# Kernel tuning notes

Measured on AMD Instinct MI355X. Metric: run time of the kernel, lower is better.

The kernel has to match this reference:

```python
import jax, jax.numpy as jnp
import numpy as np

DIM = 2048
NUM_HEADS = 16
HEAD_DIM = DIM // NUM_HEADS  # 128
ROPE_BASE = 10000.0


def setup_inputs() -> dict:
    key = jax.random.key(0)
    k1, k2, k3 = jax.random.split(key, 3)
    B, S = 2, 2048
    x = jax.random.normal(k1, (B, S, DIM), dtype=jnp.float32)
    # causal mask: 1 where allowed (k <= q), 0 elsewhere
    mask = jnp.tril(jnp.ones((S, S), dtype=jnp.int32))
    # torch Linear(dim, 3*dim, bias=False): store transposed so y = x @ w
    w_qkv = jax.random.normal(k2, (DIM, 3 * DIM), dtype=jnp.float32) / np.sqrt(DIM)
    w_out = jax.random.normal(k3, (DIM, DIM), dtype=jnp.float32) / np.sqrt(DIM)
    return {"x": x, "w_qkv": w_qkv, "w_out": w_out, "mask": mask}


def _rope_cos_sin(seq_len, dtype):
    inv_freq = 1.0 / (ROPE_BASE ** (jnp.arange(0, HEAD_DIM, 2, dtype=jnp.float32) / HEAD_DIM))
    t = jnp.arange(seq_len, dtype=jnp.float32)
    freqs = t[:, None] * inv_freq[None, :]          # [S, D/2]
    emb = jnp.concatenate([freqs, freqs], axis=-1)  # [S, D]
    return jnp.cos(emb).astype(dtype), jnp.sin(emb).astype(dtype)


def _rotate_half(x):
    x1, x2 = jnp.split(x, 2, axis=-1)
    return jnp.concatenate([-x2, x1], axis=-1)


def reference(x, w_qkv, w_out, mask):
    B, S, _ = x.shape
    H, D = NUM_HEADS, HEAD_DIM
    qkv = x @ w_qkv                                   # [B, S, 3*dim]
    qkv = qkv.reshape(B, S, 3, H, D).transpose(2, 0, 3, 1, 4)  # [3, B, H, S, D]
    q, k, v = qkv[0], qkv[1], qkv[2]
    cos, sin = _rope_cos_sin(S, x.dtype)              # [S, D] broadcast over B,H
    q = q * cos + _rotate_half(q) * sin
    k = k * cos + _rotate_half(k) * sin
    scale = D ** -0.5
    score = jnp.einsum("bhqd,bhkd->bhqk", q, k) * scale
    score = jnp.where(mask == 0, -jnp.inf, score)
    attn = jax.nn.softmax(score, axis=-1)             # dropout = identity (eval)
    out = jnp.einsum("bhqk,bhkd->bhqd", attn, v)
    out = out.transpose(0, 2, 1, 3).reshape(B, S, H * D)
    return out @ w_out
```

## Files before the change

### kernel.cpp

```cpp
#include <hip/hip_runtime.h>

typedef __attribute__((ext_vector_type(8))) __bf16 bf16x8;
typedef __attribute__((ext_vector_type(4))) float f32x4;

__device__ __forceinline__ unsigned short f2bf(float x) {
  union { float f; unsigned int u; } v; v.f = x;
  unsigned int r = v.u + 0x7fffu + ((v.u >> 16) & 1u);
  return (unsigned short)(r >> 16);
}
__device__ __forceinline__ float bf2f(unsigned short x) {
  union { unsigned int u; float f; } v; v.u = ((unsigned int)x) << 16;
  return v.f;
}
__device__ __forceinline__ void g2l16(const void* g, void* l) {
  __builtin_amdgcn_global_load_lds((const __attribute__((address_space(1))) void*)g,
                                   (__attribute__((address_space(3))) void*)l, 16, 0, 0);
}

__global__ __launch_bounds__(256) void prep_k(const float* __restrict__ x,
                                              const float* __restrict__ wq,
                                              const float* __restrict__ wo,
                                              unsigned short* __restrict__ xb,
                                              unsigned short* __restrict__ wqT,
                                              unsigned short* __restrict__ woT) {
  __shared__ unsigned short t[64][65];
  const int b = blockIdx.x;
  if (b < 8192) {
    int i = b * 256 + threadIdx.x;
    float4 v = ((const float4*)x)[i];
    ushort4 o;
    o.x = f2bf(v.x); o.y = f2bf(v.y); o.z = f2bf(v.z); o.w = f2bf(v.w);
    ((ushort4*)xb)[i] = o;
    return;
  }
  const float* in; unsigned short* out; int C, c0, r0;
  const int R = 2048;
  if (b < 11264) { int bb = b - 8192;  in = wq; out = wqT; C = 6144; c0 = (bb % 96) * 64; r0 = (bb / 96) * 64; }
  else           { int bb = b - 11264; in = wo; out = woT; C = 2048; c0 = (bb & 31) * 64; r0 = (bb >> 5) * 64; }
  const int tx = threadIdx.x & 63, tg = threadIdx.x >> 6;
#pragma unroll
  for (int i = 0; i < 16; i++) {
    int r = i * 4 + tg;
    t[r][tx] = f2bf(in[(size_t)(r0 + r) * C + c0 + tx]);
  }
  __syncthreads();
#pragma unroll
  for (int i = 0; i < 16; i++) {
    int c = i * 4 + tg;
    out[(size_t)(c0 + c) * R + r0 + tx] = t[tx][c];
  }
}

template <int EPI>
__global__ __launch_bounds__(256) void gemm_bt_k(const unsigned short* __restrict__ A,
                                                 const unsigned short* __restrict__ BT,
                                                 int K, int N,
                                                 float* __restrict__ outF,
                                                 unsigned short* __restrict__ oq,
                                                 unsigned short* __restrict__ ok,
                                                 unsigned short* __restrict__ ov) {
  __shared__ __align__(16) unsigned short smem[17408];
  unsigned short* lA = smem;
  unsigned short* lB = smem + 8192;
  const int tid = threadIdx.x;
  const int w = tid >> 6, lane = tid & 63;
  const int quad = lane >> 4, l16 = lane & 15;
  const int m0 = blockIdx.y * 128, n0 = blockIdx.x * 128;
  const int wm = (w >> 1) * 64, wn = (w & 1) * 64;
  f32x4 acc[4][4] = {};
  const int srow = tid >> 3;
  const int schunk = (tid & 7) ^ (srow & 7);
  const unsigned short* gA = A + (size_t)(m0 + srow) * K + schunk * 8;
  const unsigned short* gB = BT + (size_t)(n0 + srow) * K + schunk * 8;
  char* ldA = (char*)lA + tid * 16;
  char* ldB = (char*)lB + tid * 16;
  const size_t rskip = (size_t)32 * K;
  for (int k0 = 0; k0 < K; k0 += 64) {
#pragma unroll
    for (int j = 0; j < 4; j++) {
      g2l16(gA + k0 + j * rskip, ldA + j * 4096);
      g2l16(gB + k0 + j * rskip, ldB + j * 4096);
    }
    __syncthreads();
#pragma unroll
    for (int ks = 0; ks < 2; ks++) {
      bf16x8 af[4], bfv[4];
#pragma unroll
      for (int i = 0; i < 4; i++)
        af[i] = *(const bf16x8*)((const char*)lA + (size_t)(wm + i * 16 + l16) * 128 +
                                 ((size_t)((ks * 4 + quad) ^ (l16 & 7)) * 16));
#pragma unroll
      for (int j = 0; j < 4; j++)
        bfv[j] = *(const bf16x8*)((const char*)lB + (size_t)(wn + j * 16 + l16) * 128 +
                                  ((size_t)((ks * 4 + quad) ^ (l16 & 7)) * 16));
#pragma unroll
      for (int i = 0; i < 4; i++)
#pragma unroll
        for (int j = 0; j < 4; j++)
          acc[i][j] = __builtin_amdgcn_mfma_f32_16x16x32_bf16(af[i], bfv[j], acc[i][j], 0, 0, 0);
    }
    __syncthreads();
  }
  if (EPI == 0) {
    const int which = n0 >> 11;
    const int h = (n0 >> 7) & 15;
    const int bi2 = m0 >> 11, s0 = m0 & 2047;
    if (which < 2) {
#pragma unroll
      for (int i = 0; i < 4; i++)
#pragma unroll
        for (int r = 0; r < 4; r++) {
          int row = wm + i * 16 + quad * 4 + r;
#pragma unroll
          for (int j = 0; j < 4; j++)
            smem[row * 130 + wn + j * 16 + l16] = f2bf(acc[i][j][r]);
        }
      __syncthreads();
      unsigned short* dst = (which == 0) ? oq : ok;
      const float scale = (which == 0) ? 0.08838834764831845f : 1.0f;
      const int d = tid & 63, tg = tid >> 6;
      const float fr = exp2f(-(float)d * (13.287712379549449f / 64.0f));
      const size_t hb = ((size_t)(bi2 * 16 + h) * 2048 + s0) * 128;
#pragma unroll
      for (int i = 0; i < 32; i++) {
        int r = i * 4 + tg;
        float a = bf2f(smem[r * 130 + d]);
        float bb = bf2f(smem[r * 130 + 64 + d]);
        float sn, cs;
        __sincosf((float)(s0 + r) * fr, &sn, &cs);
        dst[hb + (size_t)r * 128 + d]      = f2bf((a * cs - bb * sn) * scale);
        dst[hb + (size_t)r * 128 + 64 + d] = f2bf((bb * cs + a * sn) * scale);
      }
    } else {
#pragma unroll
      for (int i = 0; i < 4; i++)
#pragma unroll
        for (int j = 0; j < 4; j++) {
          int row = wm + i * 16 + quad * 4;
          int col = wn + j * 16 + l16;
          ushort4 t4;
          t4.x = f2bf(acc[i][j][0]); t4.y = f2bf(acc[i][j][1]);
          t4.z = f2bf(acc[i][j][2]); t4.w = f2bf(acc[i][j][3]);
          *(ushort4*)&smem[col * 136 + row] = t4;
        }
      __syncthreads();
      const int sc = tid & 15, dbase = tid >> 4;
      const size_t vrb = ((size_t)(bi2 * 16 + h) * 128) * 2048 + s0;
#pragma unroll
      for (int v = 0; v < 8; v++) {
        int d = dbase + v * 16;
        uint4 val = *(const uint4*)&smem[d * 136 + sc * 8];
        *(uint4*)(ov + vrb + (size_t)d * 2048 + sc * 8) = val;
      }
    }
  } else {
#pragma unroll
    for (int i = 0; i < 4; i++)
#pragma unroll
      for (int r = 0; r < 4; r++) {
        size_t rowb = (size_t)(m0 + wm + i * 16 + quad * 4 + r) * N;
#pragma unroll
        for (int j = 0; j < 4; j++)
          outF[rowb + n0 + wn + j * 16 + l16] = acc[i][j][r];
      }
  }
}

__global__ __launch_bounds__(256, 2) void attn_k(const unsigned short* __restrict__ qb,
                                                 const unsigned short* __restrict__ kb,
                                                 const unsigned short* __restrict__ vt,
                                                 unsigned short* __restrict__ ob) {
  __shared__ __align__(16) unsigned short lK[64 * 128];
  __shared__ __align__(16) unsigned short lV[128 * 64];
  __shared__ __align__(16) __bf16 pbuf[4][32 * 72];
  const int tid = threadIdx.x;
  const int w = tid >> 6, lane = tid & 63;
  const int quad = lane >> 4, l16 = lane & 15;
  const int qt = (blockIdx.y < 16) ? (int)blockIdx.x : 15 - (int)blockIdx.x;
  const int bh = blockIdx.y;
  const int bi = bh >> 4, h = bh & 15;
  const int q0w = qt * 128 + w * 32;
  const unsigned short* qp = qb + (size_t)bh * 2048 * 128;
  const unsigned short* kp = kb + (size_t)bh * 2048 * 128;
  const unsigned short* vp = vt + (size_t)bh * 128 * 2048;
  __bf16* pw = pbuf[w];

  bf16x8 qf[2][4];
#pragma unroll
  for (int rg = 0; rg < 2; rg++) {
    const unsigned short* qr = qp + (size_t)(q0w + rg * 16 + l16) * 128 + quad * 8;
#pragma unroll
    for (int st = 0; st < 4; st++) qf[rg][st] = *(const bf16x8*)(qr + st * 32);
  }
  f32x4 o[2][8] = {};
  f32x4 lsum[2] = {};

  const int krow = tid >> 4;
  const int kcg = (tid & 15) ^ krow;
  const int vd = tid >> 3;
  const int vsg = (tid & 7) ^ ((tid >> 3) & 7);
  unsigned short* lKdst = lK + (size_t)tid * 8;
  unsigned short* lVdst = lV + (size_t)tid * 8;

  const int nkt = 2 * qt + 2;
  const int myNkt = (q0w + 31) / 64 + 1;
  for (int kt = 0; kt < nkt; kt++) {
    const int kt0 = kt * 64;
#pragma unroll
    for (int j = 0; j < 4; j++) {
      g2l16(kp + (size_t)(kt0 + j * 16 + krow) * 128 + kcg * 8, lKdst + j * 2048);
      g2l16(vp + (size_t)(j * 32 + vd) * 2048 + kt0 + vsg * 8, lVdst + j * 2048);
    }
    __syncthreads();
    if (kt < myNkt) {
      f32x4 sc[2][4] = {};
#pragma unroll
      for (int ct = 0; ct < 4; ct++) {
        const int nrow = ct * 16 + l16;
#pragma unroll
        for (int st = 0; st < 4; st++) {
          bf16x8 kf = *(const bf16x8*)(lK + ((size_t)nrow * 16 + ((st * 4 + quad) ^ l16)) * 8);
          sc[0][ct] = __builtin_amdgcn_mfma_f32_16x16x32_bf16(qf[0][st], kf, sc[0][ct], 0, 0, 0);
          sc[1][ct] = __builtin_amdgcn_mfma_f32_16x16x32_bf16(qf[1][st], kf, sc[1][ct], 0, 0, 0);
        }
      }
      const bool needmask = (kt == myNkt - 1);
#pragma unroll
      for (int rg = 0; rg < 2; rg++)
#pragma unroll
        for (int ct = 0; ct < 4; ct++) {
          const int col = kt0 + ct * 16 + l16;
          const int rowb = q0w + rg * 16 + quad * 4;
#pragma unroll
          for (int r = 0; r < 4; r++) {
            float s = sc[rg][ct][r];
            if (needmask && col > rowb + r) s = -1e30f;
            float e = __expf(s);
            lsum[rg][r] += e;
            pw[(rg * 16 + quad * 4 + r) * 72 + ct * 16 + l16] = (__bf16)e;
          }
        }
      bf16x8 pf[2][2];
#pragma unroll
      for (int rg = 0; rg < 2; rg++)
#pragma unroll
        for (int sb = 0; sb < 2; sb++)
          pf[rg][sb] = *(const bf16x8*)(pw + (rg * 16 + l16) * 72 + sb * 32 + quad * 8);
#pragma unroll
      for (int dt = 0; dt < 8; dt++) {
#pragma unroll
        for (int sb = 0; sb < 2; sb++) {
          bf16x8 vf = *(const bf16x8*)(lV +
              ((size_t)(dt * 16 + l16) * 8 + ((sb * 4 + quad) ^ (l16 & 7))) * 8);
          o[0][dt] = __builtin_amdgcn_mfma_f32_16x16x32_bf16(pf[0][sb], vf, o[0][dt], 0, 0, 0);
          o[1][dt] = __builtin_amdgcn_mfma_f32_16x16x32_bf16(pf[1][sb], vf, o[1][dt], 0, 0, 0);
        }
      }
    }
    __syncthreads();
  }
#pragma unroll
  for (int m = 1; m < 16; m <<= 1)
#pragma unroll
    for (int rg = 0; rg < 2; rg++)
#pragma unroll
      for (int r = 0; r < 4; r++)
        lsum[rg][r] += __shfl_xor(lsum[rg][r], m, 64);
  float inv[2][4];
#pragma unroll
  for (int rg = 0; rg < 2; rg++)
#pragma unroll
    for (int r = 0; r < 4; r++) inv[rg][r] = 1.0f / lsum[rg][r];
#pragma unroll
  for (int rg = 0; rg < 2; rg++)
#pragma unroll
    for (int dt = 0; dt < 8; dt++)
#pragma unroll
      for (int r = 0; r < 4; r++)
        ob[(size_t)(bi * 2048 + q0w + rg * 16 + quad * 4 + r) * 2048 + h * 128 + dt * 16 + l16] =
            f2bf(o[rg][dt][r] * inv[rg][r]);
}

extern "C" void kernel_launch(void* const* d_in, const int* in_sizes, int n_in,
                              void* d_out, int out_size, void* d_ws, size_t ws_size,
                              hipStream_t stream) {
  const float* x = (const float*)d_in[0];
  const float* wqkv = (const float*)d_in[1];
  const float* wout = (const float*)d_in[2];
  char* ws = (char*)d_ws;
  const size_t MiB = 1ull << 20;
  unsigned short* xb    = (unsigned short*)(ws + 0);
  unsigned short* wqkvT = (unsigned short*)(ws + 16 * MiB);
  unsigned short* woutT = (unsigned short*)(ws + 40 * MiB);
  unsigned short* qb    = (unsigned short*)(ws + 48 * MiB);
  unsigned short* kb    = (unsigned short*)(ws + 64 * MiB);
  unsigned short* vtb   = (unsigned short*)(ws + 80 * MiB);
  unsigned short* attnb = (unsigned short*)(ws + 96 * MiB);
  float* outF = (float*)d_out;

  prep_k<<<12288, 256, 0, stream>>>(x, wqkv, wout, xb, wqkvT, woutT);
  gemm_bt_k<0><<<dim3(48, 32), 256, 0, stream>>>(xb, wqkvT, 2048, 6144, nullptr, qb, kb, vtb);
  attn_k<<<dim3(16, 32), 256, 0, stream>>>(qb, kb, vtb, attnb);
  gemm_bt_k<1><<<dim3(16, 32), 256, 0, stream>>>(attnb, woutT, 2048, 2048, outF,
                                                 nullptr, nullptr, nullptr);
}
```

Before: 377.4 us.

## Replace QKV GEMM with 256x256 tile, 8-wave, multi-stage pipelined kernel

Adds a dedicated QKV projection kernel that uses 256x256 output tiles with 8 waves, a deep global-to-LDS prefetch pipeline, and explicit vmcnt waits. Barriers and setprio are interleaved with MFMA bursts. Block IDs are remapped for XCD-aware locality. The RoPE and V-transpose epilogue is redone in two chunks through shared memory. The aim is to raise MFMA utilization and data reuse over the older 128x128 kernel. The cost is a 128KB LDS footprint, heavy register pressure, and fragile hand-tuned synchronization.

```diff
diff --git a/kernel.cpp b/kernel.cpp
--- a/kernel.cpp
+++ b/kernel.cpp
@@ -16,6 +16,13 @@
   __builtin_amdgcn_global_load_lds((const __attribute__((address_space(1))) void*)g,
                                    (__attribute__((address_space(3))) void*)l, 16, 0, 0);
 }
+
+#define BARX()                                  \
+  do {                                          \
+    asm volatile("" ::: "memory");              \
+    __builtin_amdgcn_s_barrier();               \
+    asm volatile("" ::: "memory");              \
+  } while (0)
 
 __global__ __launch_bounds__(256) void prep_k(const float* __restrict__ x,
                                               const float* __restrict__ wq,
@@ -48,6 +55,176 @@
   for (int i = 0; i < 16; i++) {
     int c = i * 4 + tg;
     out[(size_t)(c0 + c) * R + r0 + tx] = t[tx][c];
+  }
+}
+
+__global__ __launch_bounds__(512, 2) void gemm8_qkv(const unsigned short* __restrict__ A,
+                                                    const unsigned short* __restrict__ BT,
+                                                    unsigned short* __restrict__ oq,
+                                                    unsigned short* __restrict__ ok,
+                                                    unsigned short* __restrict__ ov) {
+  __shared__ __align__(16) unsigned short smem8[65536];
+  const int tid = threadIdx.x;
+  const int w = tid >> 6, lane = tid & 63;
+  const int quad = lane >> 4, l16 = lane & 15;
+  const int id = (int)blockIdx.x;
+  const int wg = (id & 7) * 48 + (id >> 3);
+  const int bx = wg % 24, by = wg / 24;
+  const int m0 = by * 256, n0 = bx * 256;
+  const int wm = (w >> 2) * 128, wn = (w & 3) * 64;
+  f32x4 acc[8][4] = {};
+
+  const int rr = tid >> 3, csw = (tid & 7) ^ (rr & 7);
+  const unsigned short* gA = A + (size_t)(m0 + rr) * 2048 + csw * 8;
+  const unsigned short* gB = BT + (size_t)(n0 + rr) * 2048 + csw * 8;
+  char* ldst = (char*)smem8 + tid * 16;
+  auto STAGE = [&](int s) {
+    if (s <= 127) {
+      const int tau = s >> 2, u = s & 3, hh = u & 1;
+      char* l = ldst + ((u < 2) ? 65536 : 0) + (tau & 1) * 32768 + hh * 16384;
+      const unsigned short* g = ((u < 2) ? gB : gA) + (size_t)hh * 128 * 2048 + tau * 64;
+      g2l16(g, (void*)l);
+      g2l16(g + (size_t)64 * 2048, (void*)(l + 8192));
+    }
+  };
+
+  const char* sA = (const char*)smem8 + (wm >> 7) * 16384 + l16 * 128;
+  const char* sB = (const char*)smem8 + 65536 + (wn >> 7) * 16384 + ((wn & 64) + l16) * 128;
+  const int x0 = (quad ^ (l16 & 7)) * 16;
+  const int x1 = ((4 + quad) ^ (l16 & 7)) * 16;
+
+#define KTILE(T, PB, NV)                                                                          \
+  {                                                                                               \
+    const int _t = (T);                                                                           \
+    bf16x8 a0[4][2], bq[4][2];                                                                    \
+    _Pragma("unroll") for (int i = 0; i < 4; ++i) {                                               \
+      a0[i][0] = *(const bf16x8*)(sA + (PB) + i * 2048 + x0);                                     \
+      a0[i][1] = *(const bf16x8*)(sA + (PB) + i * 2048 + x1);                                     \
+    }                                                                                             \
+    _Pragma("unroll") for (int j = 0; j < 4; ++j) {                                               \
+      bq[j][0] = *(const bf16x8*)(sB + (PB) + j * 2048 + x0);                                     \
+      bq[j][1] = *(const bf16x8*)(sB + (PB) + j * 2048 + x1);                                     \
+    }                                                                                             \
+    STAGE(4 * _t + 7);                                                                            \
+    BARX();                                                                                       \
+    __builtin_amdgcn_s_setprio(1);                                                                \
+    _Pragma("unroll") for (int ks = 0; ks < 2; ++ks)                                              \
+      _Pragma("unroll") for (int i = 0; i < 4; ++i)                                               \
+        _Pragma("unroll") for (int j = 0; j < 2; ++j)                                             \
+          acc[i][j] = __builtin_amdgcn_mfma_f32_16x16x32_bf16(a0[i][ks], bq[j][ks], acc[i][j], 0, 0, 0); \
+    __builtin_amdgcn_s_setprio(0);                                                                \
+    BARX();                                                                                       \
+    STAGE(4 * _t + 8);                                                                            \
+    BARX();                                                                                       \
+    __builtin_amdgcn_s_setprio(1);                                                                \
+    _Pragma("unroll") for (int ks = 0; ks < 2; ++ks)                                              \
+      _Pragma("unroll") for (int i = 0; i < 4; ++i)                                               \
+        _Pragma("unroll") for (int j = 2; j < 4; ++j)                                             \
+          acc[i][j] = __builtin_amdgcn_mfma_f32_16x16x32_bf16(a0[i][ks], bq[j][ks], acc[i][j], 0, 0, 0); \
+    __builtin_amdgcn_s_setprio(0);                                                                \
+    BARX();                                                                                       \
+    bf16x8 a1[4][2];                                                                              \
+    _Pragma("unroll") for (int i = 0; i < 4; ++i) {                                               \
+      a1[i][0] = *(const bf16x8*)(sA + (PB) + (i + 4) * 2048 + x0);                               \
+      a1[i][1] = *(const bf16x8*)(sA + (PB) + (i + 4) * 2048 + x1);                               \
+    }                                                                                             \
+    STAGE(4 * _t + 9);                                                                            \
+    BARX();                                                                                       \
+    __builtin_amdgcn_s_setprio(1);                                                                \
+    _Pragma("unroll") for (int ks = 0; ks < 2; ++ks)                                              \
+      _Pragma("unroll") for (int i = 0; i < 4; ++i)                                               \
+        _Pragma("unroll") for (int j = 0; j < 2; ++j)                                             \
+          acc[i + 4][j] = __builtin_amdgcn_mfma_f32_16x16x32_bf16(a1[i][ks], bq[j][ks], acc[i + 4][j], 0, 0, 0); \
+    __builtin_amdgcn_s_setprio(0);                                                                \
+    BARX();                                                                                       \
+    STAGE(4 * _t + 10);                                                                           \
+    BARX();                                                                                       \
+    __builtin_amdgcn_s_setprio(1);                                                                \
+    _Pragma("unroll") for (int ks = 0; ks < 2; ++ks)                                              \
+      _Pragma("unroll") for (int i = 0; i < 4; ++i)                                               \
+        _Pragma("unroll") for (int j = 2; j < 4; ++j)                                             \
+          acc[i + 4][j] = __builtin_amdgcn_mfma_f32_16x16x32_bf16(a1[i][ks], bq[j][ks], acc[i + 4][j], 0, 0, 0); \
+    __builtin_amdgcn_s_setprio(0);                                                                \
+    if ((NV) == 6) asm volatile("s_waitcnt vmcnt(6)" ::: "memory");                               \
+    else if ((NV) == 0) asm volatile("s_waitcnt vmcnt(0)" ::: "memory");                          \
+    BARX();                                                                                       \
+  }
+
+  for (int s = 0; s < 7; ++s) STAGE(s);
+  asm volatile("s_waitcnt vmcnt(6)" ::: "memory");
+  BARX();
+
+  for (int t2 = 0; t2 < 32; t2 += 2) {
+    KTILE(t2, 0, (t2 == 30) ? 0 : 6);
+    KTILE(t2 + 1, 32768, (t2 + 1 == 31) ? -1 : 6);
+  }
+#undef KTILE
+
+  const int which = n0 >> 11;
+  const int h2 = (n0 >> 7) & 15;
+  const int bi2 = m0 >> 11, s0 = m0 & 2047;
+  if (which < 2) {
+    unsigned short* dst = which ? ok : oq;
+    const float scale = which ? 1.0f : 0.08838834764831845f;
+    const int d = tid & 63, tg = (tid >> 6) & 3, rh = tid >> 8;
+    const float fr = exp2f(-(float)d * (13.287712379549449f / 64.0f));
+    for (int ch = 0; ch < 2; ++ch) {
+      BARX();
+      if (((w >> 1) & 1) == ch) {
+        const int rw = w >> 2, cl = (w & 1) * 64;
+#pragma unroll
+        for (int i = 0; i < 8; ++i)
+#pragma unroll
+          for (int r = 0; r < 4; ++r) {
+            int row = i * 16 + quad * 4 + r;
+#pragma unroll
+            for (int j = 0; j < 4; ++j)
+              smem8[rw * 16640 + row * 130 + cl + j * 16 + l16] = f2bf(acc[i][j][r]);
+          }
+      }
+      BARX();
+      const int h = (h2 + ch) & 15;
+      const size_t hb = ((size_t)(bi2 * 16 + h) * 2048 + s0 + rh * 128) * 128;
+      const unsigned short* tl = smem8 + rh * 16640;
+#pragma unroll
+      for (int i = 0; i < 32; ++i) {
+        int r = i * 4 + tg;
+        float xa = bf2f(tl[r * 130 + d]);
+        float xb2 = bf2f(tl[r * 130 + 64 + d]);
+        float sn, cs;
+        __sincosf((float)(s0 + rh * 128 + r) * fr, &sn, &cs);
+        dst[hb + (size_t)r * 128 + d]      = f2bf((xa * cs - xb2 * sn) * scale);
+        dst[hb + (size_t)r * 128 + 64 + d] = f2bf((xb2 * cs + xa * sn) * scale);
+      }
+    }
+  } else {
+    const int sc = tid & 15, dbase = (tid >> 4) & 15, rh = tid >> 8;
+    for (int ch = 0; ch < 2; ++ch) {
+      BARX();
+      if (((w >> 1) & 1) == ch) {
+        const int rw = w >> 2, cl = (w & 1) * 64;
+#pragma unroll
+        for (int i = 0; i < 8; ++i)
+#pragma unroll
+          for (int j = 0; j < 4; ++j) {
+            int row = i * 16 + quad * 4;
+            int col = cl + j * 16 + l16;
+            ushort4 t4;
+            t4.x = f2bf(acc[i][j][0]); t4.y = f2bf(acc[i][j][1]);
+            t4.z = f2bf(acc[i][j][2]); t4.w = f2bf(acc[i][j][3]);
+            *(ushort4*)&smem8[rw * 17408 + col * 136 + row] = t4;
+          }
+      }
+      BARX();
+      const int h = (h2 + ch) & 15;
+      const size_t vrb = ((size_t)(bi2 * 16 + h) * 128) * 2048 + s0 + rh * 128;
+#pragma unroll
+      for (int vv = 0; vv < 8; ++vv) {
+        int dd = dbase + vv * 16;
+        uint4 val = *(const uint4*)&smem8[rh * 17408 + dd * 136 + sc * 8];
+        *(uint4*)(ov + vrb + (size_t)dd * 2048 + sc * 8) = val;
+      }
+    }
   }
 }
 
@@ -102,57 +279,6 @@
     __syncthreads();
   }
   if (EPI == 0) {
-    const int which = n0 >> 11;
-    const int h = (n0 >> 7) & 15;
-    const int bi2 = m0 >> 11, s0 = m0 & 2047;
-    if (which < 2) {
-#pragma unroll
-      for (int i = 0; i < 4; i++)
-#pragma unroll
-        for (int r = 0; r < 4; r++) {
-          int row = wm + i * 16 + quad * 4 + r;
-#pragma unroll
-          for (int j = 0; j < 4; j++)
-            smem[row * 130 + wn + j * 16 + l16] = f2bf(acc[i][j][r]);
-        }
-      __syncthreads();
-      unsigned short* dst = (which == 0) ? oq : ok;
-      const float scale = (which == 0) ? 0.08838834764831845f : 1.0f;
-      const int d = tid & 63, tg = tid >> 6;
-      const float fr = exp2f(-(float)d * (13.287712379549449f / 64.0f));
-      const size_t hb = ((size_t)(bi2 * 16 + h) * 2048 + s0) * 128;
-#pragma unroll
-      for (int i = 0; i < 32; i++) {
-        int r = i * 4 + tg;
-        float a = bf2f(smem[r * 130 + d]);
-        float bb = bf2f(smem[r * 130 + 64 + d]);
-        float sn, cs;
-        __sincosf((float)(s0 + r) * fr, &sn, &cs);
-        dst[hb + (size_t)r * 128 + d]      = f2bf((a * cs - bb * sn) * scale);
-        dst[hb + (size_t)r * 128 + 64 + d] = f2bf((bb * cs + a * sn) * scale);
-      }
-    } else {
-#pragma unroll
-      for (int i = 0; i < 4; i++)
-#pragma unroll
-        for (int j = 0; j < 4; j++) {
-          int row = wm + i * 16 + quad * 4;
-          int col = wn + j * 16 + l16;
-          ushort4 t4;
-          t4.x = f2bf(acc[i][j][0]); t4.y = f2bf(acc[i][j][1]);
-          t4.z = f2bf(acc[i][j][2]); t4.w = f2bf(acc[i][j][3]);
-          *(ushort4*)&smem[col * 136 + row] = t4;
-        }
-      __syncthreads();
-      const int sc = tid & 15, dbase = tid >> 4;
-      const size_t vrb = ((size_t)(bi2 * 16 + h) * 128) * 2048 + s0;
-#pragma unroll
-      for (int v = 0; v < 8; v++) {
-        int d = dbase + v * 16;
-        uint4 val = *(const uint4*)&smem[d * 136 + sc * 8];
-        *(uint4*)(ov + vrb + (size_t)d * 2048 + sc * 8) = val;
-      }
-    }
   } else {
 #pragma unroll
     for (int i = 0; i < 4; i++)
@@ -299,7 +425,7 @@
   float* outF = (float*)d_out;
 
   prep_k<<<12288, 256, 0, stream>>>(x, wqkv, wout, xb, wqkvT, woutT);
-  gemm_bt_k<0><<<dim3(48, 32), 256, 0, stream>>>(xb, wqkvT, 2048, 6144, nullptr, qb, kb, vtb);
+  gemm8_qkv<<<384, 512, 0, stream>>>(xb, wqkvT, qb, kb, vtb);
   attn_k<<<dim3(16, 32), 256, 0, stream>>>(qb, kb, vtb, attnb);
   gemm_bt_k<1><<<dim3(16, 32), 256, 0, stream>>>(attnb, woutT, 2048, 2048, outF,
                                                  nullptr, nullptr, nullptr);
```

Result: slower. 431.4 us (+14.3%).

## Prefetch next K and V tiles during current tile compute in attention

Applied to the files above, without the earlier changes.

Restructures the attention key loop so the next K tile load is issued right after the QK^T MFMAs and the next V tile load right after the PV MFMAs. Explicit vmcnt waits and raw s_barrier replace the full __syncthreads, so each load overlaps the other half of the compute. This hides global-to-LDS latency but adds barriers per iteration and relies on hand-tuned waitcnt ordering, which is fragile if the compiler reorders memory operations.

```diff
diff --git a/kernel.cpp b/kernel.cpp
--- a/kernel.cpp
+++ b/kernel.cpp
@@ -16,6 +16,13 @@
   __builtin_amdgcn_global_load_lds((const __attribute__((address_space(1))) void*)g,
                                    (__attribute__((address_space(3))) void*)l, 16, 0, 0);
 }
+
+#define BARX()                                  \
+  do {                                          \
+    asm volatile("" ::: "memory");              \
+    __builtin_amdgcn_s_barrier();               \
+    asm volatile("" ::: "memory");              \
+  } while (0)
 
 __global__ __launch_bounds__(256) void prep_k(const float* __restrict__ x,
                                               const float* __restrict__ wq,
@@ -204,16 +211,21 @@
 
   const int nkt = 2 * qt + 2;
   const int myNkt = (q0w + 31) / 64 + 1;
+
+#pragma unroll
+  for (int j = 0; j < 4; j++)
+    g2l16(kp + (size_t)(j * 16 + krow) * 128 + kcg * 8, lKdst + j * 2048);
+#pragma unroll
+  for (int j = 0; j < 4; j++)
+    g2l16(vp + (size_t)(j * 32 + vd) * 2048 + vsg * 8, lVdst + j * 2048);
+
   for (int kt = 0; kt < nkt; kt++) {
     const int kt0 = kt * 64;
-#pragma unroll
-    for (int j = 0; j < 4; j++) {
-      g2l16(kp + (size_t)(kt0 + j * 16 + krow) * 128 + kcg * 8, lKdst + j * 2048);
-      g2l16(vp + (size_t)(j * 32 + vd) * 2048 + kt0 + vsg * 8, lVdst + j * 2048);
-    }
-    __syncthreads();
-    if (kt < myNkt) {
-      f32x4 sc[2][4] = {};
+    asm volatile("s_waitcnt vmcnt(4)" ::: "memory");
+    BARX();
+    const bool act = (kt < myNkt);
+    f32x4 sc[2][4] = {};
+    if (act) {
 #pragma unroll
       for (int ct = 0; ct < 4; ct++) {
         const int nrow = ct * 16 + l16;
@@ -224,6 +236,15 @@
           sc[1][ct] = __builtin_amdgcn_mfma_f32_16x16x32_bf16(qf[1][st], kf, sc[1][ct], 0, 0, 0);
         }
       }
+    }
+    BARX();
+    if (kt + 1 < nkt) {
+#pragma unroll
+      for (int j = 0; j < 4; j++)
+        g2l16(kp + (size_t)(kt0 + 64 + j * 16 + krow) * 128 + kcg * 8, lKdst + j * 2048);
+    }
+    bf16x8 pf[2][2];
+    if (act) {
       const bool needmask = (kt == myNkt - 1);
 #pragma unroll
       for (int rg = 0; rg < 2; rg++)
@@ -240,12 +261,16 @@
             pw[(rg * 16 + quad * 4 + r) * 72 + ct * 16 + l16] = (__bf16)e;
           }
         }
-      bf16x8 pf[2][2];
 #pragma unroll
       for (int rg = 0; rg < 2; rg++)
 #pragma unroll
         for (int sb = 0; sb < 2; sb++)
           pf[rg][sb] = *(const bf16x8*)(pw + (rg * 16 + l16) * 72 + sb * 32 + quad * 8);
+    }
+    if (kt + 1 < nkt) asm volatile("s_waitcnt vmcnt(4)" ::: "memory");
+    else              asm volatile("s_waitcnt vmcnt(0)" ::: "memory");
+    BARX();
+    if (act) {
 #pragma unroll
       for (int dt = 0; dt < 8; dt++) {
 #pragma unroll
@@ -257,7 +282,12 @@
         }
       }
     }
-    __syncthreads();
+    BARX();
+    if (kt + 1 < nkt) {
+#pragma unroll
+      for (int j = 0; j < 4; j++)
+        g2l16(vp + (size_t)(j * 32 + vd) * 2048 + kt0 + 64 + vsg * 8, lVdst + j * 2048);
+    }
   }
 #pragma unroll
   for (int m = 1; m < 16; m <<= 1)
```

New measurement: 401.2 us. 6.3% more time.

## Double-buffer K/V tiles in attention with async prefetch; vectorize weight transpose

Applied to the files above, without the earlier changes.

The attention kernel now double-buffers its K and V tiles in LDS. The next tile is prefetched with global_load_lds while the current one is computed, and explicit vmcnt waits plus raw barriers replace __syncthreads. MFMA sections are wrapped in s_setprio, and the P buffer padding drops from 72 to 64, which may add LDS bank conflicts. Separately, the prep transpose kernel is changed to float4 loads and ushort4 stores. LDS use rises to 64KB for K/V plus the P buffers, which with 2 blocks per CU may approach the LDS limit.

```diff
diff --git a/kernel.cpp b/kernel.cpp
--- a/kernel.cpp
+++ b/kernel.cpp
@@ -16,6 +16,13 @@
   __builtin_amdgcn_global_load_lds((const __attribute__((address_space(1))) void*)g,
                                    (__attribute__((address_space(3))) void*)l, 16, 0, 0);
 }
+
+#define BARX()                                  \
+  do {                                          \
+    asm volatile("" ::: "memory");              \
+    __builtin_amdgcn_s_barrier();               \
+    asm volatile("" ::: "memory");              \
+  } while (0)
 
 __global__ __launch_bounds__(256) void prep_k(const float* __restrict__ x,
                                               const float* __restrict__ wq,
@@ -37,17 +44,26 @@
   const int R = 2048;
   if (b < 11264) { int bb = b - 8192;  in = wq; out = wqT; C = 6144; c0 = (bb % 96) * 64; r0 = (bb / 96) * 64; }
   else           { int bb = b - 11264; in = wo; out = woT; C = 2048; c0 = (bb & 31) * 64; r0 = (bb >> 5) * 64; }
-  const int tx = threadIdx.x & 63, tg = threadIdx.x >> 6;
-#pragma unroll
-  for (int i = 0; i < 16; i++) {
-    int r = i * 4 + tg;
-    t[r][tx] = f2bf(in[(size_t)(r0 + r) * C + c0 + tx]);
+  const int tx16 = threadIdx.x & 15, rr4 = threadIdx.x >> 4;
+#pragma unroll
+  for (int p = 0; p < 4; p++) {
+    const int r = p * 16 + rr4;
+    float4 v = *(const float4*)&in[(size_t)(r0 + r) * C + c0 + tx16 * 4];
+    t[r][tx16 * 4 + 0] = f2bf(v.x);
+    t[r][tx16 * 4 + 1] = f2bf(v.y);
+    t[r][tx16 * 4 + 2] = f2bf(v.z);
+    t[r][tx16 * 4 + 3] = f2bf(v.w);
   }
   __syncthreads();
 #pragma unroll
-  for (int i = 0; i < 16; i++) {
-    int c = i * 4 + tg;
-    out[(size_t)(c0 + c) * R + r0 + tx] = t[tx][c];
+  for (int p = 0; p < 4; p++) {
+    const int c = p * 16 + rr4;
+    ushort4 o4;
+    o4.x = t[tx16 * 4 + 0][c];
+    o4.y = t[tx16 * 4 + 1][c];
+    o4.z = t[tx16 * 4 + 2][c];
+    o4.w = t[tx16 * 4 + 3][c];
+    *(ushort4*)&out[(size_t)(c0 + c) * R + r0 + tx16 * 4] = o4;
   }
 }
 
@@ -170,9 +186,8 @@
                                                  const unsigned short* __restrict__ kb,
                                                  const unsigned short* __restrict__ vt,
                                                  unsigned short* __restrict__ ob) {
-  __shared__ __align__(16) unsigned short lK[64 * 128];
-  __shared__ __align__(16) unsigned short lV[128 * 64];
-  __shared__ __align__(16) __bf16 pbuf[4][32 * 72];
+  __shared__ __align__(16) unsigned short smem[32768];
+  __shared__ __align__(16) __bf16 pbuf[4][32 * 64];
   const int tid = threadIdx.x;
   const int w = tid >> 6, lane = tid & 63;
   const int quad = lane >> 4, l16 = lane & 15;
@@ -199,31 +214,49 @@
   const int kcg = (tid & 15) ^ krow;
   const int vd = tid >> 3;
   const int vsg = (tid & 7) ^ ((tid >> 3) & 7);
-  unsigned short* lKdst = lK + (size_t)tid * 8;
-  unsigned short* lVdst = lV + (size_t)tid * 8;
 
   const int nkt = 2 * qt + 2;
   const int myNkt = (q0w + 31) / 64 + 1;
+
+#pragma unroll
+  for (int j = 0; j < 4; j++) {
+    g2l16(kp + (size_t)(j * 16 + krow) * 128 + kcg * 8, smem + tid * 8 + j * 2048);
+    g2l16(vp + (size_t)(j * 32 + vd) * 2048 + vsg * 8, smem + 16384 + tid * 8 + j * 2048);
+  }
+
   for (int kt = 0; kt < nkt; kt++) {
-    const int kt0 = kt * 64;
-#pragma unroll
-    for (int j = 0; j < 4; j++) {
-      g2l16(kp + (size_t)(kt0 + j * 16 + krow) * 128 + kcg * 8, lKdst + j * 2048);
-      g2l16(vp + (size_t)(j * 32 + vd) * 2048 + kt0 + vsg * 8, lVdst + j * 2048);
-    }
-    __syncthreads();
+    const int cur = kt & 1;
+    const unsigned short* lKc = smem + cur * 8192;
+    const unsigned short* lVc = smem + 16384 + cur * 8192;
+    if (kt + 1 < nkt) {
+      unsigned short* kd = smem + (cur ^ 1) * 8192 + tid * 8;
+      unsigned short* vdd = smem + 16384 + (cur ^ 1) * 8192 + tid * 8;
+      const int kb0 = (kt + 1) * 64;
+#pragma unroll
+      for (int j = 0; j < 4; j++) {
+        g2l16(kp + (size_t)(kb0 + j * 16 + krow) * 128 + kcg * 8, kd + j * 2048);
+        g2l16(vp + (size_t)(j * 32 + vd) * 2048 + kb0 + vsg * 8, vdd + j * 2048);
+      }
+      asm volatile("s_waitcnt vmcnt(8)" ::: "memory");
+    } else {
+      asm volatile("s_waitcnt vmcnt(0)" ::: "memory");
+    }
+    BARX();
     if (kt < myNkt) {
+      const int kt0 = kt * 64;
       f32x4 sc[2][4] = {};
+      __builtin_amdgcn_s_setprio(1);
 #pragma unroll
       for (int ct = 0; ct < 4; ct++) {
         const int nrow = ct * 16 + l16;
 #pragma unroll
         for (int st = 0; st < 4; st++) {
-          bf16x8 kf = *(const bf16x8*)(lK + ((size_t)nrow * 16 + ((st * 4 + quad) ^ l16)) * 8);
+          bf16x8 kf = *(const bf16x8*)(lKc + ((size_t)nrow * 16 + ((st * 4 + quad) ^ l16)) * 8);
           sc[0][ct] = __builtin_amdgcn_mfma_f32_16x16x32_bf16(qf[0][st], kf, sc[0][ct], 0, 0, 0);
           sc[1][ct] = __builtin_amdgcn_mfma_f32_16x16x32_bf16(qf[1][st], kf, sc[1][ct], 0, 0, 0);
         }
       }
+      __builtin_amdgcn_s_setprio(0);
       const bool needmask = (kt == myNkt - 1);
 #pragma unroll
       for (int rg = 0; rg < 2; rg++)
@@ -237,7 +270,7 @@
             if (needmask && col > rowb + r) s = -1e30f;
             float e = __expf(s);
             lsum[rg][r] += e;
-            pw[(rg * 16 + quad * 4 + r) * 72 + ct * 16 + l16] = (__bf16)e;
+            pw[(rg * 16 + quad * 4 + r) * 64 + ct * 16 + l16] = (__bf16)e;
           }
         }
       bf16x8 pf[2][2];
@@ -245,19 +278,21 @@
       for (int rg = 0; rg < 2; rg++)
 #pragma unroll
         for (int sb = 0; sb < 2; sb++)
-          pf[rg][sb] = *(const bf16x8*)(pw + (rg * 16 + l16) * 72 + sb * 32 + quad * 8);
+          pf[rg][sb] = *(const bf16x8*)(pw + (rg * 16 + l16) * 64 + sb * 32 + quad * 8);
+      __builtin_amdgcn_s_setprio(1);
 #pragma unroll
       for (int dt = 0; dt < 8; dt++) {
 #pragma unroll
         for (int sb = 0; sb < 2; sb++) {
-          bf16x8 vf = *(const bf16x8*)(lV +
+          bf16x8 vf = *(const bf16x8*)(lVc +
               ((size_t)(dt * 16 + l16) * 8 + ((sb * 4 + quad) ^ (l16 & 7))) * 8);
           o[0][dt] = __builtin_amdgcn_mfma_f32_16x16x32_bf16(pf[0][sb], vf, o[0][dt], 0, 0, 0);
           o[1][dt] = __builtin_amdgcn_mfma_f32_16x16x32_bf16(pf[1][sb], vf, o[1][dt], 0, 0, 0);
         }
       }
-    }
-    __syncthreads();
+      __builtin_amdgcn_s_setprio(0);
+    }
+    BARX();
   }
 #pragma unroll
   for (int m = 1; m < 16; m <<= 1)
```

Measured after the change: 389.5 us. 3.2% more time.
